# Kernel tuning notes

Hardware: AMD Instinct MI355X
Metric: run time of the kernel (lower is better)

## Reference

```python
import jax, jax.numpy as jnp
import numpy as np
import math

N_NODES = 100000
N_EDGES = 3200000
F_IN = 512
HID = 128
N_CLS = 16


def setup_inputs() -> dict:
    key = jax.random.key(0)
    k = jax.random.split(key, 6)
    x = jax.random.normal(k[0], (N_NODES, F_IN), dtype=jnp.float32)
    edge_index = jax.random.randint(k[1], (2, N_EDGES), 0, N_NODES, dtype=jnp.int32)
    W1 = jax.random.normal(k[2], (F_IN, HID), dtype=jnp.float32) / np.sqrt(F_IN)
    W2 = jax.random.normal(k[3], (HID, HID), dtype=jnp.float32) / np.sqrt(HID)
    W3 = jax.random.normal(k[4], (N_CLS, HID), dtype=jnp.float32) / np.sqrt(HID)
    b3 = jnp.zeros((N_CLS,), dtype=jnp.float32)
    return {"x": x, "edge_index": edge_index, "W1": W1, "W2": W2, "W3": W3, "b3": b3}


def _sym_norm(edge_index, num_nodes, dtype):
    # add self loops with fill_value = trunc(log2(average_node_degree))
    E = edge_index.shape[1]
    fill = float(math.trunc(math.log2(E / num_nodes)))
    loops = jnp.arange(num_nodes, dtype=edge_index.dtype)
    row = jnp.concatenate([edge_index[0], loops])
    col = jnp.concatenate([edge_index[1], loops])
    w = jnp.concatenate([jnp.ones((E,), dtype), jnp.full((num_nodes,), fill, dtype)])
    deg = jax.ops.segment_sum(w, row, num_segments=num_nodes)
    deg_inv_sqrt = jnp.where(deg > 0, jax.lax.rsqrt(deg), 0.0)
    norm = deg_inv_sqrt[row] * w * deg_inv_sqrt[col]
    return row, col, norm


def reference(x, edge_index, W1, W2, W3, b3):
    N = x.shape[0]
    row, col, norm = _sym_norm(edge_index, N, x.dtype)

    def gcn(h, W):
        h = h @ W                                   # [N, d_out]
        msg = norm[:, None] * h[col]                # gather + scale, [E', d_out]
        return jax.ops.segment_sum(msg, row, num_segments=N)

    h = jax.nn.relu(gcn(x, W1))      # layer 1 + srelu (threshold clamped at 0)
    h = gcn(h, W2)                   # layer 2
    # dropout p=0.5 is identity in eval mode
    return h @ W3.T + b3             # linear classifier [N, n_classes]
```

## Files before the change

### kernel.cpp

```cpp
#include <hip/hip_runtime.h>
#include <cmath>

typedef __attribute__((ext_vector_type(8))) short short8;
typedef __attribute__((ext_vector_type(8))) unsigned short ushort8;
typedef __attribute__((ext_vector_type(4))) float f32x4;
typedef __attribute__((ext_vector_type(2))) float f32x2;
typedef __attribute__((ext_vector_type(4))) unsigned int uint4v;
typedef __attribute__((ext_vector_type(2))) int int2v;

#define EPB 4096
#define BCAP 20480

__device__ inline float bf16_lo(unsigned int p) {
  union { unsigned int i; float f; } v; v.i = p << 16; return v.f;
}
__device__ inline float bf16_hi(unsigned int p) {
  union { unsigned int i; float f; } v; v.i = p & 0xffff0000u; return v.f;
}
__device__ inline f32x2 bf2(unsigned int p) {
  union { unsigned int i; float f; } lo, hi;
  lo.i = p << 16;
  hi.i = p & 0xffff0000u;
  return (f32x2){lo.f, hi.f};
}
__device__ inline float bf16u(unsigned short w) {
  union { unsigned int i; float f; } v; v.i = (unsigned int)w << 16; return v.f;
}
__device__ inline unsigned short f32_to_bf16(float f) {
  union { float f; unsigned int i; } v; v.f = f;
  unsigned int x = v.i;
  x += 0x7fffu + ((x >> 16) & 1u);
  return (unsigned short)(x >> 16);
}
__device__ inline f32x2 pk_add(f32x2 a, f32x2 b) {
  f32x2 d;
  asm("v_pk_add_f32 %0, %1, %2" : "=v"(d) : "v"(a), "v"(b));
  return d;
}

__global__ __launch_bounds__(256) void bin_k(const int* __restrict__ rows,
                                             const int* __restrict__ cols,
                                             int* __restrict__ bucket_cursor,
                                             unsigned int* __restrict__ binned, int E) {
  __shared__ int lhist[256];
  __shared__ int gbase[256];
  __shared__ int loff[256];
  const int t = threadIdx.x;
  const int base = blockIdx.x * EPB;
  lhist[t] = 0;
  __syncthreads();

  int bk[16];
  unsigned int pk[16];
#pragma unroll
  for (int j = 0; j < 16; ++j) {
    int e = base + j * 256 + t;
    if (e < E) {
      int r = rows[e];
      int c = cols[e];
      bk[j] = r >> 9;
      pk[j] = ((unsigned int)(r & 511) << 17) | (unsigned int)c;
      atomicAdd(&lhist[bk[j]], 1);
    } else {
      bk[j] = -1;
    }
  }
  __syncthreads();
  if (lhist[t] > 0) gbase[t] = atomicAdd(&bucket_cursor[t], lhist[t]);
  loff[t] = 0;
  __syncthreads();
#pragma unroll
  for (int j = 0; j < 16; ++j) {
    if (bk[j] >= 0) {
      int rank = gbase[bk[j]] + atomicAdd(&loff[bk[j]], 1);
      if (rank < BCAP) binned[(size_t)bk[j] * BCAP + rank] = pk[j];
    }
  }
}

__global__ __launch_bounds__(1024) void bucket_csr_k(const unsigned int* __restrict__ binned,
                                                     const int* __restrict__ bucket_cursor,
                                                     int2v* __restrict__ rowse,
                                                     float* __restrict__ dis,
                                                     int* __restrict__ col_sorted,
                                                     int* __restrict__ perm,
                                                     int N, float fill) {
  __shared__ int lcnt[512];
  __shared__ int lscan[512];
  __shared__ int dh[512];
  __shared__ int ds2[512];
  const int b = blockIdx.x;
  const int t = threadIdx.x;
  const int start = b * BCAP;
  int cnt = bucket_cursor[b];
  if (cnt > BCAP) cnt = BCAP;
  const int endb = start + cnt;
  const int rbase = b << 9;

  if (t < 512) lcnt[t] = 0;
  __syncthreads();
  for (int i = start + t; i < endb; i += 1024)
    atomicAdd(&lcnt[binned[i] >> 17], 1);
  __syncthreads();

  int v = (t < 512) ? lcnt[t] : 0;
  if (t < 512) lscan[t] = v;
  __syncthreads();
  for (int off = 1; off < 512; off <<= 1) {
    int add = (t < 512 && t >= off) ? lscan[t - off] : 0;
    __syncthreads();
    if (t < 512) lscan[t] += add;
    __syncthreads();
  }

  if (t < 512) {
    int excl = lscan[t] - v;
    int r = rbase + t;
    if (r < N) {
      rowse[r] = (int2v){start + excl, start + excl + v};
      float d = (float)v + fill;
      dis[r] = d > 0.f ? rsqrtf(d) : 0.f;
    }
    lcnt[t] = excl;
  }

  if (t < 512) dh[t] = 0;
  __syncthreads();
  int key = 0;
  if (t < 512) {
    key = 511 - (v < 511 ? v : 511);
    atomicAdd(&dh[key], 1);
  }
  __syncthreads();
  if (t < 512) ds2[t] = dh[t];
  __syncthreads();
  for (int off = 1; off < 512; off <<= 1) {
    int add = (t < 512 && t >= off) ? ds2[t - off] : 0;
    __syncthreads();
    if (t < 512) ds2[t] += add;
    __syncthreads();
  }
  int base2 = 0;
  if (t < 512) base2 = ds2[t] - dh[t];
  __syncthreads();
  if (t < 512) dh[t] = base2;
  __syncthreads();
  if (t < 512) {
    int rank = atomicAdd(&dh[key], 1);
    perm[(b << 9) + rank] = rbase + t;
  }
  __syncthreads();

  for (int i = start + t; i < endb; i += 1024) {
    unsigned int pk = binned[i];
    int rl = (int)(pk >> 17);
    int c = (int)(pk & 0x1FFFFu);
    int pos = atomicAdd(&lcnt[rl], 1);
    col_sorted[start + pos] = c;
  }
}

__global__ __launch_bounds__(256) void cast_w_k(const float* __restrict__ W1,
                                                const float* __restrict__ W2,
                                                const float* __restrict__ W3,
                                                unsigned short* __restrict__ W1t,
                                                unsigned short* __restrict__ W2t,
                                                unsigned short* __restrict__ W3b,
                                                int FIN) {
  int g = blockIdx.x * 256 + threadIdx.x;
  int n1 = FIN * 128;
  if (g < n1) {
    int n = g & 127, k = g >> 7;
    W1t[n * FIN + k] = f32_to_bf16(W1[(size_t)k * 128 + n]);
  } else if (g < n1 + 128 * 128) {
    int gg = g - n1;
    int n = gg & 127, k = gg >> 7;
    W2t[n * 128 + k] = f32_to_bf16(W2[k * 128 + n]);
  } else if (g < n1 + 128 * 128 + 16 * 128) {
    int gg = g - n1 - 128 * 128;
    W3b[gg] = f32_to_bf16(W3[gg]);
  }
}

__global__ __launch_bounds__(256) void gemm_k(const void* __restrict__ Aq, int a_is_f32,
                                              int M, int K,
                                              const unsigned short* __restrict__ Bt,
                                              const float* __restrict__ dis,
                                              unsigned short* __restrict__ C) {
  __shared__ unsigned short Al[128 * 40];
  __shared__ unsigned short Bl[128 * 40];
  const int t = threadIdx.x;
  const int bm = blockIdx.x * 128;
  const int lane = t & 63;
  const int wave = t >> 6;
  const int wm = (wave >> 1) * 64;
  const int wn = (wave & 1) * 64;
  const int l15 = lane & 15;
  const int l4 = lane >> 4;

  f32x4 acc[4][4];
#pragma unroll
  for (int a = 0; a < 4; ++a)
#pragma unroll
    for (int b = 0; b < 4; ++b) acc[a][b] = (f32x4){0.f, 0.f, 0.f, 0.f};

  const int am = t >> 1;
  const int ak = (t & 1) * 16;
  const int bn = t >> 1;
  const int bk = (t & 1) * 16;
  const int arow = bm + am;
  const bool arow_ok = arow < M;

  auto load_a = [&](int k0, ushort8& o0, ushort8& o1) {
    o0 = (ushort8){0, 0, 0, 0, 0, 0, 0, 0};
    o1 = (ushort8){0, 0, 0, 0, 0, 0, 0, 0};
    if (arow_ok) {
      if (a_is_f32) {
        const float* p = (const float*)Aq + (size_t)arow * K + k0 + ak;
#pragma unroll
        for (int j = 0; j < 8; ++j) o0[j] = f32_to_bf16(p[j]);
#pragma unroll
        for (int j = 0; j < 8; ++j) o1[j] = f32_to_bf16(p[8 + j]);
      } else {
        const unsigned short* p = (const unsigned short*)Aq + (size_t)arow * K + k0 + ak;
        o0 = *(const ushort8*)p;
        o1 = *(const ushort8*)(p + 8);
      }
    }
  };

  ushort8 av0, av1;
  load_a(0, av0, av1);
  ushort8 bv0 = *(const ushort8*)(Bt + (size_t)bn * K + bk);
  ushort8 bv1 = *(const ushort8*)(Bt + (size_t)bn * K + bk + 8);

  for (int k0 = 0; k0 < K; k0 += 32) {
    *(ushort8*)&Al[am * 40 + ak] = av0;
    *(ushort8*)&Al[am * 40 + ak + 8] = av1;
    *(ushort8*)&Bl[bn * 40 + bk] = bv0;
    *(ushort8*)&Bl[bn * 40 + bk + 8] = bv1;
    __syncthreads();

    const int kn = k0 + 32;
    if (kn < K) {
      load_a(kn, av0, av1);
      bv0 = *(const ushort8*)(Bt + (size_t)bn * K + kn + bk);
      bv1 = *(const ushort8*)(Bt + (size_t)bn * K + kn + bk + 8);
    }

    short8 af[4];
#pragma unroll
    for (int mt = 0; mt < 4; ++mt)
      af[mt] = *(const short8*)&Al[(wm + mt * 16 + l15) * 40 + l4 * 8];
#pragma unroll
    for (int nt = 0; nt < 4; ++nt) {
      short8 bfr = *(const short8*)&Bl[(wn + nt * 16 + l15) * 40 + l4 * 8];
#pragma unroll
      for (int mt = 0; mt < 4; ++mt)
        acc[mt][nt] = __builtin_amdgcn_mfma_f32_16x16x32_bf16(af[mt], bfr, acc[mt][nt], 0, 0, 0);
    }
    __syncthreads();
  }

#pragma unroll
  for (int mt = 0; mt < 4; ++mt) {
    int rbase = bm + wm + mt * 16 + l4 * 4;
#pragma unroll
    for (int r = 0; r < 4; ++r) {
      int row = rbase + r;
      if (row < M) {
        float dr = dis[row];
#pragma unroll
        for (int nt = 0; nt < 4; ++nt) {
          int col = wn + nt * 16 + l15;
          C[(size_t)row * 128 + col] = f32_to_bf16(acc[mt][nt][r] * dr);
        }
      }
    }
  }
}

__global__ __launch_bounds__(256) void agg_k(const unsigned short* __restrict__ hs,
                                             const int2v* __restrict__ rowse,
                                             const int* __restrict__ cols,
                                             const float* __restrict__ dis,
                                             const int* __restrict__ perm,
                                             unsigned short* __restrict__ out_bf,
                                             const unsigned short* __restrict__ W3b,
                                             const float* __restrict__ b3,
                                             float* __restrict__ fcout,
                                             int N, float fill, int mode) {
  const int q = blockIdx.x * 16 + (threadIdx.x >> 4);
  const unsigned int fl = threadIdx.x & 15;
  const int rid = perm[q];
  if (rid >= N) return;
  const char* __restrict__ hsc = (const char*)hs;
  const unsigned int flo = fl << 4;

  int2v se = rowse[rid];
  int e = se.x;
  const int end = se.y;

  f32x2 a0 = {0.f, 0.f}, a1 = {0.f, 0.f}, a2 = {0.f, 0.f}, a3 = {0.f, 0.f};

  for (; e + 8 <= end; e += 8) {
    unsigned int c0 = (unsigned int)cols[e];
    unsigned int c1 = (unsigned int)cols[e + 1];
    unsigned int c2 = (unsigned int)cols[e + 2];
    unsigned int c3 = (unsigned int)cols[e + 3];
    unsigned int c4 = (unsigned int)cols[e + 4];
    unsigned int c5 = (unsigned int)cols[e + 5];
    unsigned int c6 = (unsigned int)cols[e + 6];
    unsigned int c7 = (unsigned int)cols[e + 7];
    uint4v p0 = *(const uint4v*)(hsc + ((c0 << 8) | flo));
    uint4v p1 = *(const uint4v*)(hsc + ((c1 << 8) | flo));
    uint4v p2 = *(const uint4v*)(hsc + ((c2 << 8) | flo));
    uint4v p3 = *(const uint4v*)(hsc + ((c3 << 8) | flo));
    uint4v p4 = *(const uint4v*)(hsc + ((c4 << 8) | flo));
    uint4v p5 = *(const uint4v*)(hsc + ((c5 << 8) | flo));
    uint4v p6 = *(const uint4v*)(hsc + ((c6 << 8) | flo));
    uint4v p7 = *(const uint4v*)(hsc + ((c7 << 8) | flo));
    a0 = pk_add(a0, bf2(p0[0])); a1 = pk_add(a1, bf2(p0[1]));
    a2 = pk_add(a2, bf2(p0[2])); a3 = pk_add(a3, bf2(p0[3]));
    a0 = pk_add(a0, bf2(p1[0])); a1 = pk_add(a1, bf2(p1[1]));
    a2 = pk_add(a2, bf2(p1[2])); a3 = pk_add(a3, bf2(p1[3]));
    a0 = pk_add(a0, bf2(p2[0])); a1 = pk_add(a1, bf2(p2[1]));
    a2 = pk_add(a2, bf2(p2[2])); a3 = pk_add(a3, bf2(p2[3]));
    a0 = pk_add(a0, bf2(p3[0])); a1 = pk_add(a1, bf2(p3[1]));
    a2 = pk_add(a2, bf2(p3[2])); a3 = pk_add(a3, bf2(p3[3]));
    a0 = pk_add(a0, bf2(p4[0])); a1 = pk_add(a1, bf2(p4[1]));
    a2 = pk_add(a2, bf2(p4[2])); a3 = pk_add(a3, bf2(p4[3]));
    a0 = pk_add(a0, bf2(p5[0])); a1 = pk_add(a1, bf2(p5[1]));
    a2 = pk_add(a2, bf2(p5[2])); a3 = pk_add(a3, bf2(p5[3]));
    a0 = pk_add(a0, bf2(p6[0])); a1 = pk_add(a1, bf2(p6[1]));
    a2 = pk_add(a2, bf2(p6[2])); a3 = pk_add(a3, bf2(p6[3]));
    a0 = pk_add(a0, bf2(p7[0])); a1 = pk_add(a1, bf2(p7[1]));
    a2 = pk_add(a2, bf2(p7[2])); a3 = pk_add(a3, bf2(p7[3]));
  }
  for (; e + 4 <= end; e += 4) {
    unsigned int c0 = (unsigned int)cols[e];
    unsigned int c1 = (unsigned int)cols[e + 1];
    unsigned int c2 = (unsigned int)cols[e + 2];
    unsigned int c3 = (unsigned int)cols[e + 3];
    uint4v p0 = *(const uint4v*)(hsc + ((c0 << 8) | flo));
    uint4v p1 = *(const uint4v*)(hsc + ((c1 << 8) | flo));
    uint4v p2 = *(const uint4v*)(hsc + ((c2 << 8) | flo));
    uint4v p3 = *(const uint4v*)(hsc + ((c3 << 8) | flo));
    a0 = pk_add(a0, bf2(p0[0])); a1 = pk_add(a1, bf2(p0[1]));
    a2 = pk_add(a2, bf2(p0[2])); a3 = pk_add(a3, bf2(p0[3]));
    a0 = pk_add(a0, bf2(p1[0])); a1 = pk_add(a1, bf2(p1[1]));
    a2 = pk_add(a2, bf2(p1[2])); a3 = pk_add(a3, bf2(p1[3]));
    a0 = pk_add(a0, bf2(p2[0])); a1 = pk_add(a1, bf2(p2[1]));
    a2 = pk_add(a2, bf2(p2[2])); a3 = pk_add(a3, bf2(p2[3]));
    a0 = pk_add(a0, bf2(p3[0])); a1 = pk_add(a1, bf2(p3[1]));
    a2 = pk_add(a2, bf2(p3[2])); a3 = pk_add(a3, bf2(p3[3]));
  }
  for (; e < end; ++e) {
    unsigned int c = (unsigned int)cols[e];
    uint4v p = *(const uint4v*)(hsc + ((c << 8) | flo));
    a0 = pk_add(a0, bf2(p[0])); a1 = pk_add(a1, bf2(p[1]));
    a2 = pk_add(a2, bf2(p[2])); a3 = pk_add(a3, bf2(p[3]));
  }

  uint4v ps = *(const uint4v*)(hsc + (((unsigned int)rid << 8) | flo));
  float dr = dis[rid];
  float v[8];
  v[0] = dr * (a0.x + fill * bf16_lo(ps[0]));
  v[1] = dr * (a0.y + fill * bf16_hi(ps[0]));
  v[2] = dr * (a1.x + fill * bf16_lo(ps[1]));
  v[3] = dr * (a1.y + fill * bf16_hi(ps[1]));
  v[4] = dr * (a2.x + fill * bf16_lo(ps[2]));
  v[5] = dr * (a2.y + fill * bf16_hi(ps[2]));
  v[6] = dr * (a3.x + fill * bf16_lo(ps[3]));
  v[7] = dr * (a3.y + fill * bf16_hi(ps[3]));

  if (mode == 0) {
    uint4v o;
#pragma unroll
    for (int k = 0; k < 4; ++k) {
      float f0 = fmaxf(v[2 * k], 0.f);
      float f1 = fmaxf(v[2 * k + 1], 0.f);
      o[k] = ((unsigned int)f32_to_bf16(f1) << 16) | (unsigned int)f32_to_bf16(f0);
    }
    *(uint4v*)((char*)out_bf + (((unsigned int)rid << 8) | flo)) = o;
  } else {
    float p[16];
#pragma unroll
    for (int c = 0; c < 16; ++c) {
      ushort8 wr = *(const ushort8*)(W3b + c * 128 + fl * 8);
      float s = v[0] * bf16u(wr[0]);
      s = fmaf(v[1], bf16u(wr[1]), s);
      s = fmaf(v[2], bf16u(wr[2]), s);
      s = fmaf(v[3], bf16u(wr[3]), s);
      s = fmaf(v[4], bf16u(wr[4]), s);
      s = fmaf(v[5], bf16u(wr[5]), s);
      s = fmaf(v[6], bf16u(wr[6]), s);
      s = fmaf(v[7], bf16u(wr[7]), s);
      p[c] = s;
    }
#pragma unroll
    for (int m = 1; m <= 8; m <<= 1)
#pragma unroll
      for (int c = 0; c < 16; ++c) p[c] += __shfl_xor(p[c], m);
    fcout[(size_t)rid * 16 + fl] = p[fl] + b3[fl];
  }
}

extern "C" void kernel_launch(void* const* d_in, const int* in_sizes, int n_in,
                              void* d_out, int out_size, void* d_ws, size_t ws_size,
                              hipStream_t stream) {
  const float* x  = (const float*)d_in[0];
  const int* edge = (const int*)d_in[1];
  const float* W1 = (const float*)d_in[2];
  const float* W2 = (const float*)d_in[3];
  const float* W3 = (const float*)d_in[4];
  const float* b3 = (const float*)d_in[5];
  float* out = (float*)d_out;

  const int HID = 128;
  const int FIN = in_sizes[2] / HID;
  const int N   = in_sizes[0] / FIN;
  const int E   = in_sizes[1] / 2;
  const float fill = truncf(log2f((float)E / (float)N));

  char* w = (char*)d_ws;
  size_t off = 0;
  auto alloc = [&](size_t bytes) -> void* {
    void* p = w + off;
    off += (bytes + 255) & ~(size_t)255;
    return p;
  };
  const int NB = (N + 511) >> 9;
  float* dis      = (float*)alloc((size_t)N * 4);
  int2v* rowse    = (int2v*)alloc((size_t)N * 8);
  int* perm       = (int*)alloc((size_t)NB * 512 * 4);
  int* col_sorted = (int*)alloc((size_t)NB * BCAP * 4);
  int* bucket_cursor = (int*)alloc(256 * 4);
  unsigned int* binned = (unsigned int*)alloc((size_t)NB * BCAP * 4);
  unsigned short* W1t  = (unsigned short*)alloc((size_t)FIN * 128 * 2);
  unsigned short* W2t  = (unsigned short*)alloc(128 * 128 * 2);
  unsigned short* W3b  = (unsigned short*)alloc(16 * 128 * 2);
  unsigned short* bufA = (unsigned short*)alloc((size_t)N * 128 * 2);
  unsigned short* bufB = (unsigned short*)alloc((size_t)N * 128 * 2);

  const int* rows  = edge;
  const int* colsp = edge + E;

  hipMemsetAsync(bucket_cursor, 0, 256 * 4, stream);
  bin_k<<<(E + EPB - 1) / EPB, 256, 0, stream>>>(rows, colsp, bucket_cursor, binned, E);
  bucket_csr_k<<<NB, 1024, 0, stream>>>(binned, bucket_cursor, rowse, dis,
                                        col_sorted, perm, N, fill);
  const int castN = FIN * 128 + 128 * 128 + 16 * 128;
  cast_w_k<<<(castN + 255) / 256, 256, 0, stream>>>(W1, W2, W3, W1t, W2t, W3b, FIN);

  const int gm = (N + 127) / 128;
  gemm_k<<<gm, 256, 0, stream>>>(x, 1, N, FIN, W1t, dis, bufA);
  agg_k<<<NB * 32, 256, 0, stream>>>(bufA, rowse, col_sorted, dis, perm, bufB,
                                     W3b, b3, out, N, fill, 0);
  gemm_k<<<gm, 256, 0, stream>>>(bufB, 0, N, HID, W2t, dis, bufA);
  agg_k<<<NB * 32, 256, 0, stream>>>(bufA, rowse, col_sorted, dis, perm, bufB,
                                     W3b, b3, out, N, fill, 1);
}
```

Measured before the change: 651.3 us.

## Shard hidden features into 16-column slabs for cache-local aggregation

The hidden feature buffers now use a sharded layout of eight slabs of 16 bf16 columns, written that way by the GEMM epilogue and read that way by the next GEMM. Each aggregation block handles one slab for 128 rows, two lanes per row, so the gathered working set per slab is small enough to stay in cache. The classifier moves into a separate cls_k kernel, and the bucket scans switch to wave-shuffle scans; cols, perm and rowse reads and the output stores become nontemporal. The cost is eight times as many passes over the edge list, plus one extra kernel launch and an extra pass over the final features.

```diff
diff --git a/kernel.cpp b/kernel.cpp
--- a/kernel.cpp
+++ b/kernel.cpp
@@ -10,6 +10,7 @@
 
 #define EPB 4096
 #define BCAP 20480
+#define NSH 8
 
 __device__ inline float bf16_lo(unsigned int p) {
   union { unsigned int i; float f; } v; v.i = p << 16; return v.f;
@@ -86,9 +87,8 @@
                                                      int* __restrict__ perm,
                                                      int N, float fill) {
   __shared__ int lcnt[512];
-  __shared__ int lscan[512];
   __shared__ int dh[512];
-  __shared__ int ds2[512];
+  __shared__ int wsum[16];
   const int b = blockIdx.x;
   const int t = threadIdx.x;
   const int start = b * BCAP;
@@ -97,6 +97,29 @@
   const int endb = start + cnt;
   const int rbase = b << 9;
 
+  auto scan512 = [&](int v) -> int {
+    int x = v;
+#pragma unroll
+    for (int d = 1; d < 64; d <<= 1) {
+      int u = __shfl_up(x, d, 64);
+      if ((t & 63) >= d) x += u;
+    }
+    if (t < 512 && (t & 63) == 63) wsum[t >> 6] = x;
+    __syncthreads();
+    if (t < 64) {
+      int s = (t < 8) ? wsum[t] : 0;
+#pragma unroll
+      for (int d = 1; d < 8; d <<= 1) {
+        int u = __shfl_up(s, d, 64);
+        if (t >= d) s += u;
+      }
+      if (t < 8) wsum[t] = s;
+    }
+    __syncthreads();
+    int off = (t >= 64 && t < 512) ? wsum[(t >> 6) - 1] : 0;
+    return x + off;
+  };
+
   if (t < 512) lcnt[t] = 0;
   __syncthreads();
   for (int i = start + t; i < endb; i += 1024)
@@ -104,17 +127,9 @@
   __syncthreads();
 
   int v = (t < 512) ? lcnt[t] : 0;
-  if (t < 512) lscan[t] = v;
-  __syncthreads();
-  for (int off = 1; off < 512; off <<= 1) {
-    int add = (t < 512 && t >= off) ? lscan[t - off] : 0;
-    __syncthreads();
-    if (t < 512) lscan[t] += add;
-    __syncthreads();
-  }
-
+  int incl = scan512(v);
   if (t < 512) {
-    int excl = lscan[t] - v;
+    int excl = incl - v;
     int r = rbase + t;
     if (r < N) {
       rowse[r] = (int2v){start + excl, start + excl + v};
@@ -123,6 +138,7 @@
     }
     lcnt[t] = excl;
   }
+  __syncthreads();
 
   if (t < 512) dh[t] = 0;
   __syncthreads();
@@ -132,18 +148,9 @@
     atomicAdd(&dh[key], 1);
   }
   __syncthreads();
-  if (t < 512) ds2[t] = dh[t];
-  __syncthreads();
-  for (int off = 1; off < 512; off <<= 1) {
-    int add = (t < 512 && t >= off) ? ds2[t - off] : 0;
-    __syncthreads();
-    if (t < 512) ds2[t] += add;
-    __syncthreads();
-  }
-  int base2 = 0;
-  if (t < 512) base2 = ds2[t] - dh[t];
-  __syncthreads();
-  if (t < 512) dh[t] = base2;
+  int hv = (t < 512) ? dh[t] : 0;
+  int hincl = scan512(hv);
+  if (t < 512) dh[t] = hincl - hv;
   __syncthreads();
   if (t < 512) {
     int rank = atomicAdd(&dh[key], 1);
@@ -182,8 +189,8 @@
   }
 }
 
-__global__ __launch_bounds__(256) void gemm_k(const void* __restrict__ Aq, int a_is_f32,
-                                              int M, int K,
+__global__ __launch_bounds__(256) void gemm_k(const void* __restrict__ Aq, int a_mode,
+                                              int M, int K, int SN,
                                               const unsigned short* __restrict__ Bt,
                                               const float* __restrict__ dis,
                                               unsigned short* __restrict__ C) {
@@ -215,14 +222,16 @@
     o0 = (ushort8){0, 0, 0, 0, 0, 0, 0, 0};
     o1 = (ushort8){0, 0, 0, 0, 0, 0, 0, 0};
     if (arow_ok) {
-      if (a_is_f32) {
+      if (a_mode == 0) {
         const float* p = (const float*)Aq + (size_t)arow * K + k0 + ak;
 #pragma unroll
         for (int j = 0; j < 8; ++j) o0[j] = f32_to_bf16(p[j]);
 #pragma unroll
         for (int j = 0; j < 8; ++j) o1[j] = f32_to_bf16(p[8 + j]);
       } else {
-        const unsigned short* p = (const unsigned short*)Aq + (size_t)arow * K + k0 + ak;
+        int kk = k0 + ak;
+        const unsigned short* p =
+            (const unsigned short*)Aq + ((size_t)(kk >> 4) * SN + arow) * 16;
         o0 = *(const ushort8*)p;
         o1 = *(const ushort8*)(p + 8);
       }
@@ -272,8 +281,8 @@
         float dr = dis[row];
 #pragma unroll
         for (int nt = 0; nt < 4; ++nt) {
-          int col = wn + nt * 16 + l15;
-          C[(size_t)row * 128 + col] = f32_to_bf16(acc[mt][nt][r] * dr);
+          int g = (wn >> 4) + nt;
+          C[((size_t)g * SN + row) * 16 + l15] = f32_to_bf16(acc[mt][nt][r] * dr);
         }
       }
     }
@@ -285,41 +294,45 @@
                                              const int* __restrict__ cols,
                                              const float* __restrict__ dis,
                                              const int* __restrict__ perm,
-                                             unsigned short* __restrict__ out_bf,
-                                             const unsigned short* __restrict__ W3b,
-                                             const float* __restrict__ b3,
-                                             float* __restrict__ fcout,
-                                             int N, float fill, int mode) {
-  const int q = blockIdx.x * 16 + (threadIdx.x >> 4);
-  const unsigned int fl = threadIdx.x & 15;
-  const int rid = perm[q];
+                                             unsigned short* __restrict__ out,
+                                             int SN, int N, float fill, int relu) {
+  const int b = blockIdx.x;
+  const int g = b & 7;
+  const int chunk = b >> 3;
+  const int t = threadIdx.x;
+  const unsigned int l = t & 1;
+  const int pr = t >> 1;
+  const int q = chunk * 128 + pr;
+  const int rid = __builtin_nontemporal_load(&perm[q]);
   if (rid >= N) return;
-  const char* __restrict__ hsc = (const char*)hs;
-  const unsigned int flo = fl << 4;
-
-  int2v se = rowse[rid];
+
+  const char* __restrict__ shp = (const char*)hs + (size_t)g * SN * 32;
+  char* __restrict__ shpo = (char*)out + (size_t)g * SN * 32;
+  const unsigned int lo = l << 4;
+
+  int2v se = __builtin_nontemporal_load(&rowse[rid]);
   int e = se.x;
   const int end = se.y;
 
   f32x2 a0 = {0.f, 0.f}, a1 = {0.f, 0.f}, a2 = {0.f, 0.f}, a3 = {0.f, 0.f};
 
   for (; e + 8 <= end; e += 8) {
-    unsigned int c0 = (unsigned int)cols[e];
-    unsigned int c1 = (unsigned int)cols[e + 1];
-    unsigned int c2 = (unsigned int)cols[e + 2];
-    unsigned int c3 = (unsigned int)cols[e + 3];
-    unsigned int c4 = (unsigned int)cols[e + 4];
-    unsigned int c5 = (unsigned int)cols[e + 5];
-    unsigned int c6 = (unsigned int)cols[e + 6];
-    unsigned int c7 = (unsigned int)cols[e + 7];
-    uint4v p0 = *(const uint4v*)(hsc + ((c0 << 8) | flo));
-    uint4v p1 = *(const uint4v*)(hsc + ((c1 << 8) | flo));
-    uint4v p2 = *(const uint4v*)(hsc + ((c2 << 8) | flo));
-    uint4v p3 = *(const uint4v*)(hsc + ((c3 << 8) | flo));
-    uint4v p4 = *(const uint4v*)(hsc + ((c4 << 8) | flo));
-    uint4v p5 = *(const uint4v*)(hsc + ((c5 << 8) | flo));
-    uint4v p6 = *(const uint4v*)(hsc + ((c6 << 8) | flo));
-    uint4v p7 = *(const uint4v*)(hsc + ((c7 << 8) | flo));
+    unsigned int c0 = (unsigned int)__builtin_nontemporal_load(&cols[e]);
+    unsigned int c1 = (unsigned int)__builtin_nontemporal_load(&cols[e + 1]);
+    unsigned int c2 = (unsigned int)__builtin_nontemporal_load(&cols[e + 2]);
+    unsigned int c3 = (unsigned int)__builtin_nontemporal_load(&cols[e + 3]);
+    unsigned int c4 = (unsigned int)__builtin_nontemporal_load(&cols[e + 4]);
+    unsigned int c5 = (unsigned int)__builtin_nontemporal_load(&cols[e + 5]);
+    unsigned int c6 = (unsigned int)__builtin_nontemporal_load(&cols[e + 6]);
+    unsigned int c7 = (unsigned int)__builtin_nontemporal_load(&cols[e + 7]);
+    uint4v p0 = *(const uint4v*)(shp + ((c0 << 5) | lo));
+    uint4v p1 = *(const uint4v*)(shp + ((c1 << 5) | lo));
+    uint4v p2 = *(const uint4v*)(shp + ((c2 << 5) | lo));
+    uint4v p3 = *(const uint4v*)(shp + ((c3 << 5) | lo));
+    uint4v p4 = *(const uint4v*)(shp + ((c4 << 5) | lo));
+    uint4v p5 = *(const uint4v*)(shp + ((c5 << 5) | lo));
+    uint4v p6 = *(const uint4v*)(shp + ((c6 << 5) | lo));
+    uint4v p7 = *(const uint4v*)(shp + ((c7 << 5) | lo));
     a0 = pk_add(a0, bf2(p0[0])); a1 = pk_add(a1, bf2(p0[1]));
     a2 = pk_add(a2, bf2(p0[2])); a3 = pk_add(a3, bf2(p0[3]));
     a0 = pk_add(a0, bf2(p1[0])); a1 = pk_add(a1, bf2(p1[1]));
@@ -337,32 +350,14 @@
     a0 = pk_add(a0, bf2(p7[0])); a1 = pk_add(a1, bf2(p7[1]));
     a2 = pk_add(a2, bf2(p7[2])); a3 = pk_add(a3, bf2(p7[3]));
   }
-  for (; e + 4 <= end; e += 4) {
-    unsigned int c0 = (unsigned int)cols[e];
-    unsigned int c1 = (unsigned int)cols[e + 1];
-    unsigned int c2 = (unsigned int)cols[e + 2];
-    unsigned int c3 = (unsigned int)cols[e + 3];
-    uint4v p0 = *(const uint4v*)(hsc + ((c0 << 8) | flo));
-    uint4v p1 = *(const uint4v*)(hsc + ((c1 << 8) | flo));
-    uint4v p2 = *(const uint4v*)(hsc + ((c2 << 8) | flo));
-    uint4v p3 = *(const uint4v*)(hsc + ((c3 << 8) | flo));
-    a0 = pk_add(a0, bf2(p0[0])); a1 = pk_add(a1, bf2(p0[1]));
-    a2 = pk_add(a2, bf2(p0[2])); a3 = pk_add(a3, bf2(p0[3]));
-    a0 = pk_add(a0, bf2(p1[0])); a1 = pk_add(a1, bf2(p1[1]));
-    a2 = pk_add(a2, bf2(p1[2])); a3 = pk_add(a3, bf2(p1[3]));
-    a0 = pk_add(a0, bf2(p2[0])); a1 = pk_add(a1, bf2(p2[1]));
-    a2 = pk_add(a2, bf2(p2[2])); a3 = pk_add(a3, bf2(p2[3]));
-    a0 = pk_add(a0, bf2(p3[0])); a1 = pk_add(a1, bf2(p3[1]));
-    a2 = pk_add(a2, bf2(p3[2])); a3 = pk_add(a3, bf2(p3[3]));
-  }
   for (; e < end; ++e) {
-    unsigned int c = (unsigned int)cols[e];
-    uint4v p = *(const uint4v*)(hsc + ((c << 8) | flo));
+    unsigned int c = (unsigned int)__builtin_nontemporal_load(&cols[e]);
+    uint4v p = *(const uint4v*)(shp + ((c << 5) | lo));
     a0 = pk_add(a0, bf2(p[0])); a1 = pk_add(a1, bf2(p[1]));
     a2 = pk_add(a2, bf2(p[2])); a3 = pk_add(a3, bf2(p[3]));
   }
 
-  uint4v ps = *(const uint4v*)(hsc + (((unsigned int)rid << 8) | flo));
+  uint4v ps = *(const uint4v*)(shp + (((unsigned int)rid << 5) | lo));
   float dr = dis[rid];
   float v[8];
   v[0] = dr * (a0.x + fill * bf16_lo(ps[0]));
@@ -374,36 +369,48 @@
   v[6] = dr * (a3.x + fill * bf16_lo(ps[3]));
   v[7] = dr * (a3.y + fill * bf16_hi(ps[3]));
 
-  if (mode == 0) {
-    uint4v o;
-#pragma unroll
-    for (int k = 0; k < 4; ++k) {
-      float f0 = fmaxf(v[2 * k], 0.f);
-      float f1 = fmaxf(v[2 * k + 1], 0.f);
-      o[k] = ((unsigned int)f32_to_bf16(f1) << 16) | (unsigned int)f32_to_bf16(f0);
-    }
-    *(uint4v*)((char*)out_bf + (((unsigned int)rid << 8) | flo)) = o;
-  } else {
-    float p[16];
-#pragma unroll
-    for (int c = 0; c < 16; ++c) {
-      ushort8 wr = *(const ushort8*)(W3b + c * 128 + fl * 8);
-      float s = v[0] * bf16u(wr[0]);
-      s = fmaf(v[1], bf16u(wr[1]), s);
-      s = fmaf(v[2], bf16u(wr[2]), s);
-      s = fmaf(v[3], bf16u(wr[3]), s);
-      s = fmaf(v[4], bf16u(wr[4]), s);
-      s = fmaf(v[5], bf16u(wr[5]), s);
-      s = fmaf(v[6], bf16u(wr[6]), s);
-      s = fmaf(v[7], bf16u(wr[7]), s);
-      p[c] = s;
-    }
-#pragma unroll
-    for (int m = 1; m <= 8; m <<= 1)
-#pragma unroll
-      for (int c = 0; c < 16; ++c) p[c] += __shfl_xor(p[c], m);
-    fcout[(size_t)rid * 16 + fl] = p[fl] + b3[fl];
-  }
+  uint4v o;
+#pragma unroll
+  for (int k = 0; k < 4; ++k) {
+    float f0 = v[2 * k], f1 = v[2 * k + 1];
+    if (relu) { f0 = fmaxf(f0, 0.f); f1 = fmaxf(f1, 0.f); }
+    o[k] = ((unsigned int)f32_to_bf16(f1) << 16) | (unsigned int)f32_to_bf16(f0);
+  }
+  __builtin_nontemporal_store(o, (uint4v*)(shpo + (((unsigned int)rid << 5) | lo)));
+}
+
+__global__ __launch_bounds__(256) void cls_k(const unsigned short* __restrict__ h,
+                                             const unsigned short* __restrict__ W3b,
+                                             const float* __restrict__ b3,
+                                             float* __restrict__ fcout,
+                                             int SN, int N) {
+  const int r = blockIdx.x * 16 + (threadIdx.x >> 4);
+  const unsigned int fl = threadIdx.x & 15;
+  if (r >= N) return;
+  ushort8 hv = *(const ushort8*)(h + ((size_t)(fl >> 1) * SN + r) * 16 + (fl & 1) * 8);
+  float v[8];
+#pragma unroll
+  for (int j = 0; j < 8; ++j) v[j] = bf16u(hv[j]);
+
+  float p[16];
+#pragma unroll
+  for (int c = 0; c < 16; ++c) {
+    ushort8 wr = *(const ushort8*)(W3b + c * 128 + fl * 8);
+    float s = v[0] * bf16u(wr[0]);
+    s = fmaf(v[1], bf16u(wr[1]), s);
+    s = fmaf(v[2], bf16u(wr[2]), s);
+    s = fmaf(v[3], bf16u(wr[3]), s);
+    s = fmaf(v[4], bf16u(wr[4]), s);
+    s = fmaf(v[5], bf16u(wr[5]), s);
+    s = fmaf(v[6], bf16u(wr[6]), s);
+    s = fmaf(v[7], bf16u(wr[7]), s);
+    p[c] = s;
+  }
+#pragma unroll
+  for (int m = 1; m <= 8; m <<= 1)
+#pragma unroll
+    for (int c = 0; c < 16; ++c) p[c] += __shfl_xor(p[c], m);
+  fcout[(size_t)r * 16 + fl] = p[fl] + b3[fl];
 }
 
 extern "C" void kernel_launch(void* const* d_in, const int* in_sizes, int n_in,
@@ -454,10 +461,12 @@
   cast_w_k<<<(castN + 255) / 256, 256, 0, stream>>>(W1, W2, W3, W1t, W2t, W3b, FIN);
 
   const int gm = (N + 127) / 128;
-  gemm_k<<<gm, 256, 0, stream>>>(x, 1, N, FIN, W1t, dis, bufA);
-  agg_k<<<NB * 32, 256, 0, stream>>>(bufA, rowse, col_sorted, dis, perm, bufB,
-                                     W3b, b3, out, N, fill, 0);
-  gemm_k<<<gm, 256, 0, stream>>>(bufB, 0, N, HID, W2t, dis, bufA);
-  agg_k<<<NB * 32, 256, 0, stream>>>(bufA, rowse, col_sorted, dis, perm, bufB,
-                                     W3b, b3, out, N, fill, 1);
-}
+  const int aggGrid = NB * 4 * 8;
+  gemm_k<<<gm, 256, 0, stream>>>(x, 0, N, FIN, N, W1t, dis, bufA);
+  agg_k<<<aggGrid, 256, 0, stream>>>(bufA, rowse, col_sorted, dis, perm, bufB,
+                                     N, N, fill, 1);
+  gemm_k<<<gm, 256, 0, stream>>>(bufB, 1, N, HID, N, W2t, dis, bufA);
+  agg_k<<<aggGrid, 256, 0, stream>>>(bufA, rowse, col_sorted, dis, perm, bufB,
+                                     N, N, fill, 0);
+  cls_k<<<(N + 15) / 16, 256, 0, stream>>>(bufB, W3b, b3, out, N, N);
+}
```

Result: slower. 1.044 ms (+60.2%).
